# Kernel tuning notes

Hardware: AMD Instinct MI355X
Metric: run time of the kernel (lower is better)

Reference implementation:

```python
import jax, jax.numpy as jnp
import numpy as np

EMBED = 1024
FF = 4096
LN_EPS = 1e-5

def _layernorm(x, gamma, beta):
    mu = jnp.mean(x, axis=-1, keepdims=True)
    var = jnp.var(x, axis=-1, keepdims=True)
    return (x - mu) * jax.lax.rsqrt(var + LN_EPS) * gamma + beta

def setup_inputs() -> dict:
    key = jax.random.key(0)
    ks = jax.random.split(key, 16)
    s = 1.0 / np.sqrt(EMBED)
    s2 = 1.0 / np.sqrt(FF)
    return {
        "x": jax.random.normal(ks[0], (8, 2048, EMBED), dtype=jnp.float32),
        "Wq": jax.random.uniform(ks[1], (EMBED, EMBED), jnp.float32, -s, s),
        "bq": jnp.zeros((EMBED,), jnp.float32),
        "Wk": jax.random.uniform(ks[2], (EMBED, EMBED), jnp.float32, -s, s),
        "bk": jnp.zeros((EMBED,), jnp.float32),
        "Wv": jax.random.uniform(ks[3], (EMBED, EMBED), jnp.float32, -s, s),
        "bv": jnp.zeros((EMBED,), jnp.float32),
        "Wo": jax.random.uniform(ks[4], (EMBED, EMBED), jnp.float32, -s, s),
        "bo": jnp.zeros((EMBED,), jnp.float32),
        "g1": jnp.ones((EMBED,), jnp.float32),
        "b1": jnp.zeros((EMBED,), jnp.float32),
        "g2": jnp.ones((EMBED,), jnp.float32),
        "b2": jnp.zeros((EMBED,), jnp.float32),
        "W1": jax.random.uniform(ks[5], (EMBED, FF), jnp.float32, -s, s),
        "bf1": jnp.zeros((FF,), jnp.float32),
        "W2": jax.random.uniform(ks[6], (FF, EMBED), jnp.float32, -s2, s2),
        "bf2": jnp.zeros((EMBED,), jnp.float32),
    }

def reference(x, Wq, bq, Wk, bk, Wv, bv, Wo, bo, g1, b1, g2, b2, W1, bf1, W2, bf2):
    # Single-head attention (heads arg unused in original forward)
    Q = jnp.einsum('bse,ef->bsf', x, Wq) + bq
    K = jnp.einsum('bse,ef->bsf', x, Wk) + bk
    V = jnp.einsum('bse,ef->bsf', x, Wv) + bv
    scale = 1.0 / jnp.sqrt(jnp.float32(EMBED))
    scores = jnp.einsum('bqe,bke->bqk', Q, K) * scale  # [B,S,S]
    attn = jax.nn.softmax(scores, axis=-1)
    attn_out = jnp.einsum('bqk,bke->bqe', attn, V)
    attn_out = jnp.einsum('bse,ef->bsf', attn_out, Wo) + bo
    # dropout is identity in eval mode
    h = _layernorm(x + attn_out, g1, b1)
    ffn = jnp.einsum('bsf,fh->bsh', jax.nn.relu(jnp.einsum('bse,eh->bsh', h, W1) + bf1), W2) + bf2
    return _layernorm(h + ffn, g2, b2)
```

## Files before the change

kernel.cpp:

```cpp
#include <hip/hip_runtime.h>


typedef __attribute__((ext_vector_type(4))) float  f32x4;
typedef __attribute__((ext_vector_type(8))) short  s16x8;
typedef __attribute__((ext_vector_type(4))) short  s16x4;
typedef unsigned short u16;
typedef unsigned int   u32;

__device__ __forceinline__ float bf2f(short s) {
  u32 u = ((u32)(u16)s) << 16;
  float f; __builtin_memcpy(&f, &u, 4); return f;
}
__device__ __forceinline__ short f2bf(float f) {
  u32 u; __builtin_memcpy(&u, &f, 4);
  u32 r = (u + 0x7fffu + ((u >> 16) & 1u)) >> 16;
  return (short)(u16)r;
}

__device__ __forceinline__ void gload16(const void* g, void* l) {
  __builtin_amdgcn_global_load_lds(
      (const __attribute__((address_space(1))) u32*)g,
      (__attribute__((address_space(3))) u32*)l, 16, 0, 0);
}


__device__ __forceinline__ void stage_half(const char* gop, long long ldb,
                                           long long rowbase, int tt, int h,
                                           u16* ldsop, int tid) {
#pragma unroll
  for (int l = 0; l < 2; ++l) {
    const int o   = (l * 512 + tid) * 16;
    const int rih = o >> 7;
    const int scb = (o & 127) ^ ((rih & 7) << 4);
    gload16(gop + (rowbase + h * 128 + rih) * ldb + (long long)tt * 128 + scb,
            (char*)ldsop + h * 16384 + o);
  }
}

#define RD_A(MH) do { _Pragma("unroll") for (int mi = 0; mi < 4; ++mi) { \
    const int row_ = wm * 64 + (MH) * 128 + mi * 16 + lr; \
    const int sw_ = (row_ & 7) << 4; const int rb_ = row_ << 7; \
    _Pragma("unroll") for (int kk = 0; kk < 2; ++kk) \
      af[mi][kk] = *(const s16x8*)(pa + rb_ + (((kk << 6) | (kg << 4)) ^ sw_)); } } while (0)

#define RD_B(NH) do { _Pragma("unroll") for (int nj = 0; nj < 2; ++nj) { \
    const int row_ = wn * 32 + (NH) * 128 + nj * 16 + lr; \
    const int sw_ = (row_ & 7) << 4; const int rb_ = row_ << 7; \
    _Pragma("unroll") for (int kk = 0; kk < 2; ++kk) \
      bf[NH][nj][kk] = *(const s16x8*)(pb + rb_ + (((kk << 6) | (kg << 4)) ^ sw_)); } } while (0)

#define MM(MH, NH) do { _Pragma("unroll") for (int kk = 0; kk < 2; ++kk) \
    _Pragma("unroll") for (int mi = 0; mi < 4; ++mi) \
    _Pragma("unroll") for (int nj = 0; nj < 2; ++nj) \
      acc[(MH) * 4 + mi][(NH) * 2 + nj] = __builtin_amdgcn_mfma_f32_16x16x32_bf16( \
        af[mi][kk], bf[NH][nj][kk], acc[(MH) * 4 + mi][(NH) * 2 + nj], 0, 0, 0); } while (0)

#define PH_SYNC do { __builtin_amdgcn_s_barrier(); \
    asm volatile("s_waitcnt lgkmcnt(0)"); \
    __builtin_amdgcn_sched_barrier(0); } while (0)

template<bool HAS_BIAS, bool RELU>
__global__ __launch_bounds__(512, 2)
void gemm256(const u16* __restrict__ A, const u16* __restrict__ BT,
             u16* __restrict__ C, const float* __restrict__ bias,
             int M, int N, int K, float scale,
             long long sA, long long sB, long long sC) {
  __shared__ u16 SA[2][16384];
  __shared__ u16 SB[2][16384];

  const int gx = gridDim.x, gy = gridDim.y;
  const int nwg = gx * gy * gridDim.z;
  const int orig = (blockIdx.z * gy + blockIdx.y) * gx + blockIdx.x;
  const int q = nwg >> 3, r8 = nwg & 7;
  const int xcd = orig & 7, pos = orig >> 3;
  const int wg = (xcd < r8 ? xcd * (q + 1) : r8 * (q + 1) + (xcd - r8) * q) + pos;
  const int bz = wg / (gx * gy);
  const int rem = wg % (gx * gy);
  const long long bm = (long long)(rem / gx) * 256;
  const long long bn = (long long)(rem % gx) * 256;

  const char* Ag = (const char*)(A + (long long)bz * sA);
  const char* Bg = (const char*)(BT + (long long)bz * sB);
  u16* Cb = C + (long long)bz * sC;
  const long long ldb = (long long)K * 2;

  const int tid = threadIdx.x;
  const int lane = tid & 63, wid = tid >> 6;
  const int lr = lane & 15, kg = lane >> 4;
  const int wm = wid >> 2, wn = wid & 3;
  const int NT = K >> 6;

  f32x4 acc[8][4] = {};
  s16x8 af[4][2];
  s16x8 bf[2][2][2];

  stage_half(Ag, ldb, bm, 0, 0, SA[0], tid);
  stage_half(Bg, ldb, bn, 0, 0, SB[0], tid);
  stage_half(Ag, ldb, bm, 0, 1, SA[0], tid);
  stage_half(Bg, ldb, bn, 0, 1, SB[0], tid);
  stage_half(Ag, ldb, bm, 1, 0, SA[1], tid);
  stage_half(Bg, ldb, bn, 1, 0, SB[1], tid);
  asm volatile("s_waitcnt vmcnt(4)");
  __builtin_amdgcn_s_barrier();

  for (int T = 0; T < NT; ++T) {
    const int c = T & 1, cn = c ^ 1;
    const char* pa = (const char*)SA[c];
    const char* pb = (const char*)SB[c];

    RD_A(0); RD_B(0);
    if (T + 1 < NT) stage_half(Ag, ldb, bm, T + 1, 1, SA[cn], tid);
    PH_SYNC;
    __builtin_amdgcn_s_setprio(1); MM(0, 0); __builtin_amdgcn_s_setprio(0);
    __builtin_amdgcn_s_barrier();

    RD_B(1);
    if (T + 1 < NT) stage_half(Bg, ldb, bn, T + 1, 1, SB[cn], tid);
    PH_SYNC;
    __builtin_amdgcn_s_setprio(1); MM(0, 1); __builtin_amdgcn_s_setprio(0);
    __builtin_amdgcn_s_barrier();

    RD_A(1);
    if (T + 2 < NT) stage_half(Ag, ldb, bm, T + 2, 0, SA[c], tid);
    PH_SYNC;
    __builtin_amdgcn_s_setprio(1); MM(1, 0); __builtin_amdgcn_s_setprio(0);
    __builtin_amdgcn_s_barrier();

    if (T + 2 < NT) stage_half(Bg, ldb, bn, T + 2, 0, SB[c], tid);
    PH_SYNC;
    __builtin_amdgcn_s_setprio(1); MM(1, 1); __builtin_amdgcn_s_setprio(0);
    if (T + 2 < NT)      { asm volatile("s_waitcnt vmcnt(4)"); }
    else if (T + 1 < NT) { asm volatile("s_waitcnt vmcnt(0)"); }
    __builtin_amdgcn_s_barrier();
  }

#pragma unroll
  for (int nh = 0; nh < 2; ++nh)
#pragma unroll
    for (int nj = 0; nj < 2; ++nj) {
      const long long col = bn + wn * 32 + nh * 128 + nj * 16 + lr;
      float bv = 0.f;
      if (HAS_BIAS) bv = bias[col];
#pragma unroll
      for (int mh = 0; mh < 2; ++mh)
#pragma unroll
        for (int mi = 0; mi < 4; ++mi) {
          const long long row0 = bm + wm * 64 + mh * 128 + mi * 16 + kg * 4;
#pragma unroll
          for (int r = 0; r < 4; ++r) {
            float v = acc[mh * 4 + mi][nh * 2 + nj][r] * scale + bv;
            if (RELU) v = fmaxf(v, 0.f);
            Cb[(row0 + r) * (long long)N + col] = (u16)f2bf(v);
          }
        }
    }
}

__global__ __launch_bounds__(256) void cast_f32_bf16(const float* __restrict__ in,
                                                     u16* __restrict__ out) {
  long long i = (long long)blockIdx.x * 256 + threadIdx.x;
  f32x4 v = ((const f32x4*)in)[i];
  s16x4 o;
#pragma unroll
  for (int j = 0; j < 4; j++) o[j] = f2bf(v[j]);
  ((s16x4*)out)[i] = o;
}

__global__ __launch_bounds__(256) void transpose_f32_bf16(const float* __restrict__ in,
                                                          u16* __restrict__ out,
                                                          int R, int C) {
  __shared__ float tile[32][33];
  const int tx = threadIdx.x, ty = threadIdx.y;
  const int r0 = blockIdx.y * 32, c0 = blockIdx.x * 32;
#pragma unroll
  for (int i = 0; i < 32; i += 8)
    tile[ty + i][tx] = in[(long long)(r0 + ty + i) * C + (c0 + tx)];
  __syncthreads();
#pragma unroll
  for (int i = 0; i < 32; i += 8)
    out[(long long)(c0 + ty + i) * R + (r0 + tx)] = (u16)f2bf(tile[tx][ty + i]);
}

__global__ __launch_bounds__(256) void transpose_bf16_bf16(const u16* __restrict__ in,
                                                           u16* __restrict__ out,
                                                           int R, int C,
                                                           long long isb, long long osb) {
  __shared__ u16 tile[32][33];
  in  += (long long)blockIdx.z * isb;
  out += (long long)blockIdx.z * osb;
  const int tx = threadIdx.x, ty = threadIdx.y;
  const int r0 = blockIdx.y * 32, c0 = blockIdx.x * 32;
#pragma unroll
  for (int i = 0; i < 32; i += 8)
    tile[ty + i][tx] = in[(long long)(r0 + ty + i) * C + (c0 + tx)];
  __syncthreads();
#pragma unroll
  for (int i = 0; i < 32; i += 8)
    out[(long long)(c0 + ty + i) * R + (r0 + tx)] = tile[tx][ty + i];
}

__global__ __launch_bounds__(256) void softmax2048(u16* __restrict__ S) {
  const long long row = blockIdx.x;
  u16* p = S + row * 2048;
  const int t = threadIdx.x;
  s16x8 raw = *(const s16x8*)&p[t * 8];
  float v[8];
#pragma unroll
  for (int j = 0; j < 8; j++) v[j] = bf2f(raw[j]);

  float m = -1e30f;
#pragma unroll
  for (int j = 0; j < 8; j++) m = fmaxf(m, v[j]);
#pragma unroll
  for (int off = 32; off > 0; off >>= 1) m = fmaxf(m, __shfl_xor(m, off));
  __shared__ float red[8];
  if ((t & 63) == 0) red[t >> 6] = m;
  __syncthreads();
  m = fmaxf(fmaxf(red[0], red[1]), fmaxf(red[2], red[3]));

  float s = 0.f;
#pragma unroll
  for (int j = 0; j < 8; j++) { v[j] = __expf(v[j] - m); s += v[j]; }
#pragma unroll
  for (int off = 32; off > 0; off >>= 1) s += __shfl_xor(s, off);
  if ((t & 63) == 0) red[4 + (t >> 6)] = s;
  __syncthreads();
  s = (red[4] + red[5]) + (red[6] + red[7]);

  const float inv = 1.0f / s;
  s16x8 o;
#pragma unroll
  for (int j = 0; j < 8; j++) o[j] = f2bf(v[j] * inv);
  *(s16x8*)&p[t * 8] = o;
}

__global__ __launch_bounds__(256) void ln_add_f32bf16(const float* __restrict__ x,
                                                      const u16* __restrict__ a,
                                                      const float* __restrict__ g,
                                                      const float* __restrict__ be,
                                                      u16* __restrict__ out) {
  const long long row = blockIdx.x;
  const int t = threadIdx.x;
  f32x4 xv = ((const f32x4*)(x + row * 1024))[t];
  s16x4 av = ((const s16x4*)(a + row * 1024))[t];
  float v[4]; float sum = 0.f, ss = 0.f;
#pragma unroll
  for (int j = 0; j < 4; j++) { v[j] = xv[j] + bf2f(av[j]); sum += v[j]; ss += v[j] * v[j]; }
#pragma unroll
  for (int off = 32; off > 0; off >>= 1) { sum += __shfl_xor(sum, off); ss += __shfl_xor(ss, off); }
  __shared__ float red[8];
  if ((t & 63) == 0) { red[t >> 6] = sum; red[4 + (t >> 6)] = ss; }
  __syncthreads();
  sum = (red[0] + red[1]) + (red[2] + red[3]);
  ss  = (red[4] + red[5]) + (red[6] + red[7]);
  const float mu   = sum * (1.f / 1024.f);
  const float var  = ss * (1.f / 1024.f) - mu * mu;
  const float rstd = rsqrtf(var + 1e-5f);
  s16x4 o;
#pragma unroll
  for (int j = 0; j < 4; j++) {
    const int c = t * 4 + j;
    o[j] = f2bf((v[j] - mu) * rstd * g[c] + be[c]);
  }
  *(s16x4*)&out[row * 1024 + t * 4] = o;
}

__global__ __launch_bounds__(256) void ln_add_bf16bf16(const u16* __restrict__ h,
                                                       const u16* __restrict__ f,
                                                       const float* __restrict__ g,
                                                       const float* __restrict__ be,
                                                       float* __restrict__ out) {
  const long long row = blockIdx.x;
  const int t = threadIdx.x;
  s16x4 hv = ((const s16x4*)(h + row * 1024))[t];
  s16x4 fv = ((const s16x4*)(f + row * 1024))[t];
  float v[4]; float sum = 0.f, ss = 0.f;
#pragma unroll
  for (int j = 0; j < 4; j++) { v[j] = bf2f(hv[j]) + bf2f(fv[j]); sum += v[j]; ss += v[j] * v[j]; }
#pragma unroll
  for (int off = 32; off > 0; off >>= 1) { sum += __shfl_xor(sum, off); ss += __shfl_xor(ss, off); }
  __shared__ float red[8];
  if ((t & 63) == 0) { red[t >> 6] = sum; red[4 + (t >> 6)] = ss; }
  __syncthreads();
  sum = (red[0] + red[1]) + (red[2] + red[3]);
  ss  = (red[4] + red[5]) + (red[6] + red[7]);
  const float mu   = sum * (1.f / 1024.f);
  const float var  = ss * (1.f / 1024.f) - mu * mu;
  const float rstd = rsqrtf(var + 1e-5f);
  f32x4 o;
#pragma unroll
  for (int j = 0; j < 4; j++) {
    const int c = t * 4 + j;
    o[j] = (v[j] - mu) * rstd * g[c] + be[c];
  }
  ((f32x4*)(out + row * 1024))[t] = o;
}

extern "C" void kernel_launch(void* const* d_in, const int* in_sizes, int n_in,
                              void* d_out, int out_size, void* d_ws, size_t ws_size,
                              hipStream_t stream) {
  const float* x   = (const float*)d_in[0];
  const float* Wq  = (const float*)d_in[1];
  const float* bq  = (const float*)d_in[2];
  const float* Wk  = (const float*)d_in[3];
  const float* bk  = (const float*)d_in[4];
  const float* Wv  = (const float*)d_in[5];
  const float* bv  = (const float*)d_in[6];
  const float* Wo  = (const float*)d_in[7];
  const float* bo  = (const float*)d_in[8];
  const float* g1  = (const float*)d_in[9];
  const float* b1  = (const float*)d_in[10];
  const float* g2  = (const float*)d_in[11];
  const float* b2  = (const float*)d_in[12];
  const float* W1  = (const float*)d_in[13];
  const float* bf1 = (const float*)d_in[14];
  const float* W2  = (const float*)d_in[15];
  const float* bf2 = (const float*)d_in[16];
  float* out = (float*)d_out;

  char* ws = (char*)d_ws;
  u16* wsWQT = (u16*)(ws + 0);
  u16* wsWKT = (u16*)(ws + 2097152);
  u16* wsWVT = (u16*)(ws + 4194304);
  u16* wsWOT = (u16*)(ws + 6291456);
  u16* wsW1T = (u16*)(ws + 8388608);
  u16* wsW2T = (u16*)(ws + 16777216);
  u16* wsXB  = (u16*)(ws + 25165824);
  u16* wsQ   = (u16*)(ws + 58720256);
  u16* wsK   = (u16*)(ws + 92274688);
  u16* wsV   = (u16*)(ws + 125829120);
  u16* wsVT  = (u16*)(ws + 159383552);
  u16* wsS   = (u16*)(ws + 192937984);
  u16* wsAO  = wsXB;
  u16* wsAO2 = wsQ;
  u16* wsH   = wsK;
  u16* wsHID = wsV;
  u16* wsFFN = wsXB;

  const dim3 tb(32, 8, 1);
  const float inv_sqrt_e = 0.03125f;

  cast_f32_bf16<<<16384, 256, 0, stream>>>(x, wsXB);

  transpose_f32_bf16<<<dim3(32, 32, 1),  tb, 0, stream>>>(Wq, wsWQT, 1024, 1024);
  transpose_f32_bf16<<<dim3(32, 32, 1),  tb, 0, stream>>>(Wk, wsWKT, 1024, 1024);
  transpose_f32_bf16<<<dim3(32, 32, 1),  tb, 0, stream>>>(Wv, wsWVT, 1024, 1024);
  transpose_f32_bf16<<<dim3(32, 32, 1),  tb, 0, stream>>>(Wo, wsWOT, 1024, 1024);
  transpose_f32_bf16<<<dim3(128, 32, 1), tb, 0, stream>>>(W1, wsW1T, 1024, 4096);
  transpose_f32_bf16<<<dim3(32, 128, 1), tb, 0, stream>>>(W2, wsW2T, 4096, 1024);

  gemm256<true, false><<<dim3(4, 64, 1), 512, 0, stream>>>(wsXB, wsWQT, wsQ, bq, 16384, 1024, 1024, 1.f, 0, 0, 0);
  gemm256<true, false><<<dim3(4, 64, 1), 512, 0, stream>>>(wsXB, wsWKT, wsK, bk, 16384, 1024, 1024, 1.f, 0, 0, 0);
  gemm256<true, false><<<dim3(4, 64, 1), 512, 0, stream>>>(wsXB, wsWVT, wsV, bv, 16384, 1024, 1024, 1.f, 0, 0, 0);

  transpose_bf16_bf16<<<dim3(32, 64, 8), tb, 0, stream>>>(wsV, wsVT, 2048, 1024, 2048LL * 1024, 1024LL * 2048);

  gemm256<false, false><<<dim3(8, 8, 8), 512, 0, stream>>>(wsQ, wsK, wsS, nullptr, 2048, 2048, 1024, inv_sqrt_e,
                                                           2048LL * 1024, 2048LL * 1024, 2048LL * 2048);
  softmax2048<<<16384, 256, 0, stream>>>(wsS);

  gemm256<false, false><<<dim3(4, 8, 8), 512, 0, stream>>>(wsS, wsVT, wsAO, nullptr, 2048, 1024, 2048, 1.f,
                                                           2048LL * 2048, 1024LL * 2048, 2048LL * 1024);
  gemm256<true, false><<<dim3(4, 64, 1), 512, 0, stream>>>(wsAO, wsWOT, wsAO2, bo, 16384, 1024, 1024, 1.f, 0, 0, 0);

  ln_add_f32bf16<<<16384, 256, 0, stream>>>(x, wsAO2, g1, b1, wsH);

  gemm256<true, true><<<dim3(16, 64, 1), 512, 0, stream>>>(wsH, wsW1T, wsHID, bf1, 16384, 4096, 1024, 1.f, 0, 0, 0);

  gemm256<true, false><<<dim3(4, 64, 1), 512, 0, stream>>>(wsHID, wsW2T, wsFFN, bf2, 16384, 1024, 4096, 1.f, 0, 0, 0);

  ln_add_bf16bf16<<<16384, 256, 0, stream>>>(wsH, wsFFN, g2, b2, out);

  (void)in_sizes; (void)n_in; (void)out_size; (void)ws_size;
}
```

Measured before the change: 701.6 us.

## Fuse QKV projections and fold softmax exp/normalize into attention GEMM epilogues

The three Q/K/V projection GEMMs become one launch over the contiguous transposed weight block. The epilogue routes each column range to its own output buffer and bias. Softmax is split up: the QK^T GEMM writes exp(score*scale) directly, a light kernel computes per-row reciprocal sums, and the PV GEMM scales its output rows by those reciprocals. This removes the full read-modify-write pass over the score matrix and some kernel launches, but it drops the max subtraction, so it can overflow if scores are large.

```diff
diff --git a/kernel.cpp b/kernel.cpp
--- a/kernel.cpp
+++ b/kernel.cpp
@@ -59,10 +59,12 @@
     asm volatile("s_waitcnt lgkmcnt(0)"); \
     __builtin_amdgcn_sched_barrier(0); } while (0)
 
-template<bool HAS_BIAS, bool RELU>
+template<int MODE>
 __global__ __launch_bounds__(512, 2)
 void gemm256(const u16* __restrict__ A, const u16* __restrict__ BT,
-             u16* __restrict__ C, const float* __restrict__ bias,
+             u16* __restrict__ C,
+             const float* __restrict__ bias0, const float* __restrict__ bias1,
+             const float* __restrict__ bias2, const float* __restrict__ linv,
              int M, int N, int K, float scale,
              long long sA, long long sB, long long sC) {
   __shared__ u16 SA[2][16384];
@@ -139,8 +141,16 @@
 #pragma unroll
     for (int nj = 0; nj < 2; ++nj) {
       const long long col = bn + wn * 32 + nh * 128 + nj * 16 + lr;
+      u16* outp = Cb;
+      long long ccol = col, ldc = N;
       float bv = 0.f;
-      if (HAS_BIAS) bv = bias[col];
+      if (MODE == 1 || MODE == 2) bv = bias0[col];
+      if (MODE == 5) {
+        const int sel = (int)(col >> 10);
+        outp = C + (long long)sel * 16777216;
+        ccol = col & 1023; ldc = 1024;
+        bv = (sel == 0 ? bias0 : sel == 1 ? bias1 : bias2)[ccol];
+      }
 #pragma unroll
       for (int mh = 0; mh < 2; ++mh)
 #pragma unroll
@@ -148,9 +158,12 @@
           const long long row0 = bm + wm * 64 + mh * 128 + mi * 16 + kg * 4;
 #pragma unroll
           for (int r = 0; r < 4; ++r) {
-            float v = acc[mh * 4 + mi][nh * 2 + nj][r] * scale + bv;
-            if (RELU) v = fmaxf(v, 0.f);
-            Cb[(row0 + r) * (long long)N + col] = (u16)f2bf(v);
+            float v = acc[mh * 4 + mi][nh * 2 + nj][r];
+            if (MODE == 1 || MODE == 2 || MODE == 5) v = v * scale + bv;
+            if (MODE == 2) v = fmaxf(v, 0.f);
+            if (MODE == 3) v = __expf(v * scale);
+            if (MODE == 4) v = v * linv[row0 + r];
+            outp[(row0 + r) * ldc + ccol] = (u16)f2bf(v);
           }
         }
     }
@@ -199,39 +212,24 @@
     out[(long long)(c0 + ty + i) * R + (r0 + tx)] = tile[tx][ty + i];
 }
 
-__global__ __launch_bounds__(256) void softmax2048(u16* __restrict__ S) {
+__global__ __launch_bounds__(256) void rowinv2048(const u16* __restrict__ P,
+                                                  float* __restrict__ linv) {
   const long long row = blockIdx.x;
-  u16* p = S + row * 2048;
+  const u16* p = P + row * 2048;
   const int t = threadIdx.x;
   s16x8 raw = *(const s16x8*)&p[t * 8];
-  float v[8];
-#pragma unroll
-  for (int j = 0; j < 8; j++) v[j] = bf2f(raw[j]);
-
-  float m = -1e30f;
-#pragma unroll
-  for (int j = 0; j < 8; j++) m = fmaxf(m, v[j]);
-#pragma unroll
-  for (int off = 32; off > 0; off >>= 1) m = fmaxf(m, __shfl_xor(m, off));
-  __shared__ float red[8];
-  if ((t & 63) == 0) red[t >> 6] = m;
-  __syncthreads();
-  m = fmaxf(fmaxf(red[0], red[1]), fmaxf(red[2], red[3]));
-
   float s = 0.f;
 #pragma unroll
-  for (int j = 0; j < 8; j++) { v[j] = __expf(v[j] - m); s += v[j]; }
+  for (int j = 0; j < 8; j++) s += bf2f(raw[j]);
 #pragma unroll
   for (int off = 32; off > 0; off >>= 1) s += __shfl_xor(s, off);
-  if ((t & 63) == 0) red[4 + (t >> 6)] = s;
-  __syncthreads();
-  s = (red[4] + red[5]) + (red[6] + red[7]);
-
-  const float inv = 1.0f / s;
-  s16x8 o;
-#pragma unroll
-  for (int j = 0; j < 8; j++) o[j] = f2bf(v[j] * inv);
-  *(s16x8*)&p[t * 8] = o;
+  __shared__ float red[4];
+  if ((t & 63) == 0) red[t >> 6] = s;
+  __syncthreads();
+  if (t == 0) {
+    s = (red[0] + red[1]) + (red[2] + red[3]);
+    linv[row] = 1.0f / s;
+  }
 }
 
 __global__ __launch_bounds__(256) void ln_add_f32bf16(const float* __restrict__ x,
@@ -336,9 +334,11 @@
   u16* wsH   = wsK;
   u16* wsHID = wsV;
   u16* wsFFN = wsXB;
+  float* wsLINV = (float*)wsQ;
 
   const dim3 tb(32, 8, 1);
   const float inv_sqrt_e = 0.03125f;
+  const float* nf = nullptr;
 
   cast_f32_bf16<<<16384, 256, 0, stream>>>(x, wsXB);
 
@@ -349,25 +349,29 @@
   transpose_f32_bf16<<<dim3(128, 32, 1), tb, 0, stream>>>(W1, wsW1T, 1024, 4096);
   transpose_f32_bf16<<<dim3(32, 128, 1), tb, 0, stream>>>(W2, wsW2T, 4096, 1024);
 
-  gemm256<true, false><<<dim3(4, 64, 1), 512, 0, stream>>>(wsXB, wsWQT, wsQ, bq, 16384, 1024, 1024, 1.f, 0, 0, 0);
-  gemm256<true, false><<<dim3(4, 64, 1), 512, 0, stream>>>(wsXB, wsWKT, wsK, bk, 16384, 1024, 1024, 1.f, 0, 0, 0);
-  gemm256<true, false><<<dim3(4, 64, 1), 512, 0, stream>>>(wsXB, wsWVT, wsV, bv, 16384, 1024, 1024, 1.f, 0, 0, 0);
+  gemm256<5><<<dim3(12, 64, 1), 512, 0, stream>>>(wsXB, wsWQT, wsQ, bq, bk, bv, nf,
+                                                  16384, 3072, 1024, 1.f, 0, 0, 0);
 
   transpose_bf16_bf16<<<dim3(32, 64, 8), tb, 0, stream>>>(wsV, wsVT, 2048, 1024, 2048LL * 1024, 1024LL * 2048);
 
-  gemm256<false, false><<<dim3(8, 8, 8), 512, 0, stream>>>(wsQ, wsK, wsS, nullptr, 2048, 2048, 1024, inv_sqrt_e,
-                                                           2048LL * 1024, 2048LL * 1024, 2048LL * 2048);
-  softmax2048<<<16384, 256, 0, stream>>>(wsS);
-
-  gemm256<false, false><<<dim3(4, 8, 8), 512, 0, stream>>>(wsS, wsVT, wsAO, nullptr, 2048, 1024, 2048, 1.f,
-                                                           2048LL * 2048, 1024LL * 2048, 2048LL * 1024);
-  gemm256<true, false><<<dim3(4, 64, 1), 512, 0, stream>>>(wsAO, wsWOT, wsAO2, bo, 16384, 1024, 1024, 1.f, 0, 0, 0);
+  gemm256<3><<<dim3(8, 8, 8), 512, 0, stream>>>(wsQ, wsK, wsS, nf, nf, nf, nf,
+                                                2048, 2048, 1024, inv_sqrt_e,
+                                                2048LL * 1024, 2048LL * 1024, 2048LL * 2048);
+  rowinv2048<<<16384, 256, 0, stream>>>(wsS, wsLINV);
+
+  gemm256<4><<<dim3(4, 8, 8), 512, 0, stream>>>(wsS, wsVT, wsAO, nf, nf, nf, wsLINV,
+                                                2048, 1024, 2048, 1.f,
+                                                2048LL * 2048, 1024LL * 2048, 2048LL * 1024);
+  gemm256<1><<<dim3(4, 64, 1), 512, 0, stream>>>(wsAO, wsWOT, wsAO2, bo, nf, nf, nf,
+                                                 16384, 1024, 1024, 1.f, 0, 0, 0);
 
   ln_add_f32bf16<<<16384, 256, 0, stream>>>(x, wsAO2, g1, b1, wsH);
 
-  gemm256<true, true><<<dim3(16, 64, 1), 512, 0, stream>>>(wsH, wsW1T, wsHID, bf1, 16384, 4096, 1024, 1.f, 0, 0, 0);
-
-  gemm256<true, false><<<dim3(4, 64, 1), 512, 0, stream>>>(wsHID, wsW2T, wsFFN, bf2, 16384, 1024, 4096, 1.f, 0, 0, 0);
+  gemm256<2><<<dim3(16, 64, 1), 512, 0, stream>>>(wsH, wsW1T, wsHID, bf1, nf, nf, nf,
+                                                  16384, 4096, 1024, 1.f, 0, 0, 0);
+
+  gemm256<1><<<dim3(4, 64, 1), 512, 0, stream>>>(wsHID, wsW2T, wsFFN, bf2, nf, nf, nf,
+                                                 16384, 1024, 4096, 1.f, 0, 0, 0);
 
   ln_add_bf16bf16<<<16384, 256, 0, stream>>>(wsH, wsFFN, g2, b2, out);
 
```

Measured after the change: 683.1 us. 1.03x faster.
